# Kernel optimization log

Hardware: AMD Instinct MI355X
Metric: run time of the kernel (lower is better)

## Reference

```python
import jax, jax.numpy as jnp
import numpy as np

N = 50000
E = 800000
IN_C = 64
OUT_C = 64
EPS = 1 + 1e-06


def setup_inputs() -> dict:
    key = jax.random.key(0)
    ks = jax.random.split(key, 10)
    x = jax.random.normal(ks[0], (N, IN_C), dtype=jnp.float32)
    lower_indices = jax.random.randint(ks[1], (2, E), 0, N, dtype=jnp.int64)
    lower_values = jax.random.uniform(ks[2], (E,), dtype=jnp.float32)
    upper_indices = jax.random.randint(ks[3], (2, E), 0, N, dtype=jnp.int64)
    upper_values = jax.random.uniform(ks[4], (E,), dtype=jnp.float32)
    s = 1.0 / np.sqrt(IN_C)
    w_lower = jax.random.uniform(ks[5], (IN_C, OUT_C), jnp.float32, -s, s)
    a_lower = jax.random.uniform(ks[6], (2 * OUT_C,), jnp.float32, -s, s)
    w_upper = jax.random.uniform(ks[7], (IN_C, OUT_C), jnp.float32, -s, s)
    a_upper = jax.random.uniform(ks[8], (2 * OUT_C,), jnp.float32, -s, s)
    w_lin = jax.random.uniform(ks[9], (IN_C, OUT_C), jnp.float32, -s, s)
    return {
        "x": x,
        "lower_indices": lower_indices,
        "lower_values": lower_values,
        "upper_indices": upper_indices,
        "upper_values": upper_values,
        "w_lower": w_lower,
        "a_lower": a_lower,
        "w_upper": w_upper,
        "a_upper": a_upper,
        "w_lin": w_lin,
    }


def _att_conv(x, weight, att_w, indices, values):
    """TopoModelX base Conv with att=True.

    x_msg = x @ weight; per edge (i=target, j=source):
      alpha_e = elu(concat(x_msg[j], x_msg[i]) @ att_w) * nbhd_vals_e
    out[i] = sum_e alpha_e * x_msg[j]
    """
    xm = x @ weight                              # [N, out]
    i, j = indices[0], indices[1]                # target, source
    # concat(src, tgt) @ a == src @ a[:F] + tgt @ a[F:]; precompute per-node
    s_src = xm @ att_w[:OUT_C]                   # [N]
    s_tgt = xm @ att_w[OUT_C:]                   # [N]
    alpha = jax.nn.elu(s_src[j] + s_tgt[i]) * values   # [E]
    msg = alpha[:, None] * xm[j]                 # [E, out]
    return jax.ops.segment_sum(msg, i, num_segments=N)


def reference(x, lower_indices, lower_values, upper_indices, upper_values,
              w_lower, a_lower, w_upper, a_upper, w_lin):
    lower_x = _att_conv(x, w_lower, a_lower, lower_indices, lower_values)
    upper_x = _att_conv(x, w_upper, a_upper, upper_indices, upper_values)
    w_x = (x @ w_lin) * EPS
    # Aggregation(aggr_func='sum', update_func='relu')
    return jax.nn.relu(lower_x + upper_x + w_x)
```

## Files before the change

### kernel.cpp

```cpp
#include <hip/hip_runtime.h>
#include <hip/hip_bf16.h>
#include <math.h>

#define N_NODES 50000
#define N_EDGES 800000
#define C 64
#define EPS_F 1.000001f

#define CAPN 48
#define OVF_IDX 0
#define OMAX 4096
#define LOVF 64

#define RB_BITS 7
#define RBUK (1 << RB_BITS)
#define NBUCK (2 * N_NODES)
#define NREG ((NBUCK + RBUK - 1) >> RB_BITS)
#define RCAP 2560
#define EPB 4096
#define NP1 392
#define NPREB 784
#define NK1 (3 * NP1)

#define ZERON (1 + NREG)

typedef __attribute__((ext_vector_type(8))) unsigned short u16x8;

__device__ __forceinline__ unsigned short f2bf(float f) {
    unsigned u = __float_as_uint(f);
    return (unsigned short)((u + 0x7FFFu + ((u >> 16) & 1u)) >> 16);
}
__device__ __forceinline__ float bf2f(unsigned short b) {
    return __uint_as_float(((unsigned)b) << 16);
}

__global__ __launch_bounds__(512) void gemm_scatter_kernel(
    const float* __restrict__ x,
    const float* __restrict__ w_l, const float* __restrict__ a_l,
    const float* __restrict__ w_u, const float* __restrict__ a_u,
    const float* __restrict__ w_lin,
    const int* __restrict__ lidx, const float* __restrict__ lval,
    const int* __restrict__ uidx, const float* __restrict__ uval,
    unsigned short* __restrict__ xm_l, unsigned short* __restrict__ xm_u,
    float* __restrict__ xlin,
    float* __restrict__ ssl, float* __restrict__ stl,
    float* __restrict__ ssu, float* __restrict__ stu,
    int* __restrict__ cnt, uint2* __restrict__ rbuf, int2* __restrict__ ovf)
{
    const int b = blockIdx.x, t = threadIdx.x;
    __shared__ int hist[NREG];

    if (b % 3 == 0) {
        const int p = b / 3;
        int* __restrict__ rcur = cnt + 1;

        for (int s0 = t; s0 < NREG; s0 += 512) hist[s0] = 0;
        __syncthreads();

        unsigned lo[8];
        int bk[8];
        const int gbase = p * EPB + t;
#pragma unroll
        for (int k = 0; k < 8; ++k) {
            const int g = gbase + k * 512;
            bk[k] = -1;
            if (g < 2 * N_EDGES) {
                int i, j;
                float v;
                if (g < N_EDGES) {
                    i = lidx[g]; j = lidx[N_EDGES + g]; v = lval[g];
                    bk[k] = 2 * i;
                } else {
                    const int e = g - N_EDGES;
                    i = uidx[e]; j = uidx[N_EDGES + e]; v = uval[e];
                    bk[k] = 2 * i + 1;
                }
                lo[k] = ((unsigned)j << 16) | (unsigned)f2bf(v);
                atomicAdd(&hist[bk[k] >> RB_BITS], 1);
            }
        }
        __syncthreads();

        for (int cb = t; cb < NREG; cb += 512) {
            const int c = hist[cb];
            hist[cb] = c ? atomicAdd(&rcur[cb], c) : 0;
        }
        __syncthreads();

#pragma unroll
        for (int k = 0; k < 8; ++k) {
            if (bk[k] >= 0) {
                const int cb = bk[k] >> RB_BITS;
                const int slot = atomicAdd(&hist[cb], 1);
                if (slot < RCAP) {
                    rbuf[(size_t)cb * RCAP + slot] = make_uint2(lo[k], (unsigned)bk[k]);
                } else {
                    const int oi = atomicAdd(&cnt[OVF_IDX], 1);
                    if (oi < OMAX) ovf[oi] = make_int2(bk[k], (int)lo[k]);
                }
            }
        }
        return;
    }

    const int pid = b - b / 3 - 1;
    const int lane = t & 63;
    const int wvu = __builtin_amdgcn_readfirstlane(t >> 6);
    const int row0 = pid * 64 + wvu * 8;
    if (row0 >= N_NODES) return;

    const float* xr[8];
#pragma unroll
    for (int r = 0; r < 8; ++r) {
        int rr = row0 + r;
        if (rr >= N_NODES) rr = N_NODES - 1;
        xr[r] = x + (size_t)rr * C;
    }

    float acc_l[8] = {0,0,0,0,0,0,0,0};
    float acc_u[8] = {0,0,0,0,0,0,0,0};
    float acc_n[8] = {0,0,0,0,0,0,0,0};

#pragma unroll 1
    for (int kc = 0; kc < C; kc += 4) {
#pragma unroll
        for (int kk = 0; kk < 4; ++kk) {
            const int k = kc + kk;
            const float wl = w_l[k * C + lane];
            const float wu = w_u[k * C + lane];
            const float wn = w_lin[k * C + lane];
#pragma unroll
            for (int r = 0; r < 8; ++r) {
                const float xk = xr[r][k];
                acc_l[r] = fmaf(xk, wl, acc_l[r]);
                acc_u[r] = fmaf(xk, wu, acc_u[r]);
                acc_n[r] = fmaf(xk, wn, acc_n[r]);
            }
        }
    }

    const float als = a_l[lane], alt = a_l[C + lane];
    const float aus = a_u[lane], aut = a_u[C + lane];

#pragma unroll
    for (int r = 0; r < 8; ++r) {
        const int row = row0 + r;
        if (row < N_NODES) {
            xm_l[row * C + lane] = f2bf(acc_l[r]);
            xm_u[row * C + lane] = f2bf(acc_u[r]);
            xlin[row * C + lane] = acc_n[r] * EPS_F;

            float psl = acc_l[r] * als, ptl = acc_l[r] * alt;
            float psu = acc_u[r] * aus, ptu = acc_u[r] * aut;
#pragma unroll
            for (int o = 32; o >= 1; o >>= 1) {
                psl += __shfl_xor(psl, o);
                ptl += __shfl_xor(ptl, o);
                psu += __shfl_xor(psu, o);
                ptu += __shfl_xor(ptu, o);
            }
            if (lane == 0) {
                ssl[row] = psl; stl[row] = ptl;
                ssu[row] = psu; stu[row] = ptu;
            }
        }
    }
}

__global__ __launch_bounds__(512) void gather_kernel(
    const float* __restrict__ xlin,
    const int* __restrict__ cnt, const uint2* __restrict__ rbuf,
    const int2* __restrict__ ovf,
    const unsigned short* __restrict__ xm_l, const unsigned short* __restrict__ xm_u,
    const float* __restrict__ ssl, const float* __restrict__ stl,
    const float* __restrict__ ssu, const float* __restrict__ stu,
    float* __restrict__ out)
{
    const int cb = blockIdx.x;
    const int t = threadIdx.x;
    const int wv = t >> 6, lane = t & 63;
    const int sub8 = lane >> 3;
    const int cg = lane & 7;

    __shared__ unsigned lists[RBUK * CAPN];
    __shared__ int cur[RBUK];
    __shared__ int lovf_bk[LOVF];
    __shared__ unsigned lovf_rc[LOVF];
    __shared__ int lc;

    for (int s0 = t; s0 < RBUK; s0 += 512) cur[s0] = 0;
    if (t == 0) lc = 0;
    __syncthreads();

    const int n = min(cnt[1 + cb], RCAP);
    const uint2* __restrict__ rb = rbuf + (size_t)cb * RCAP;
    for (int r = t; r < n; r += 512) {
        const uint2 e = rb[r];
        const int local = (int)e.y & (RBUK - 1);
        const int rank = atomicAdd(&cur[local], 1);
        if (rank < CAPN) {
            lists[local * CAPN + rank] = e.x;
        } else {
            const int o = atomicAdd(&lc, 1);
            if (o < LOVF) { lovf_bk[o] = local; lovf_rc[o] = e.x; }
        }
    }
    __syncthreads();

    const int oc = min(cnt[OVF_IDX], OMAX);
    const int lc2 = min(lc, LOVF);

#pragma unroll 1
    for (int p = 0; p < 8; ++p) {
        const int q = wv * 8 + p;
        const int node = cb * 64 + q;
        if (node >= N_NODES) break;
        const int lA = 2 * q, lB = 2 * q + 1;
        const int lenA = min(cur[lA], CAPN);
        const int lenB = min(cur[lB], CAPN);
        const unsigned* __restrict__ lstA = lists + lA * CAPN;
        const unsigned* __restrict__ lstB = lists + lB * CAPN;

        const float stlN = stl[node];
        const float stuN = stu[node];

        float acc[8] = {0.f,0.f,0.f,0.f,0.f,0.f,0.f,0.f};
        int kA = 0, kB = 0;
        while ((kA < lenA) | (kB < lenB)) {
            const int iA = kA + sub8, iB = kB + sub8;
            const bool aA = iA < lenA, aB = iB < lenB;
            const unsigned rwA = lstA[aA ? iA : kA];
            const unsigned rwB = lstB[aB ? iB : kB];
            const int jA = aA ? (int)(rwA >> 16) : 0;
            const int jB = aB ? (int)(rwB >> 16) : 0;
            const float vA = aA ? bf2f((unsigned short)(rwA & 0xFFFFu)) : 0.f;
            const float vB = aB ? bf2f((unsigned short)(rwB & 0xFFFFu)) : 0.f;
            const float sA = ssl[jA] + stlN;
            const float sB = ssu[jB] + stuN;
            const float eA = (sA > 0.f) ? sA : expm1f(sA);
            const float eB = (sB > 0.f) ? sB : expm1f(sB);
            const float wA = eA * vA;
            const float wB = eB * vB;
            const u16x8 rowA = *(const u16x8*)(xm_l + jA * C + cg * 8);
            const u16x8 rowB = *(const u16x8*)(xm_u + jB * C + cg * 8);
#pragma unroll
            for (int c = 0; c < 8; ++c)
                acc[c] = fmaf(wA, bf2f(rowA[c]), acc[c]);
#pragma unroll
            for (int c = 0; c < 8; ++c)
                acc[c] = fmaf(wB, bf2f(rowB[c]), acc[c]);
            kA += (kA < lenA) ? 8 : 0;
            kB += (kB < lenB) ? 8 : 0;
        }

        for (int u = 0; u < oc; ++u) {
            const int2 e = ovf[u];
            if (e.x == 2 * node || e.x == 2 * node + 1) {
                const unsigned rw = (unsigned)e.y;
                const int j = (int)(rw >> 16);
                const float v = bf2f((unsigned short)(rw & 0xFFFFu));
                const int cv = e.x & 1;
                const float s = (cv ? ssu[j] : ssl[j]) + (cv ? stuN : stlN);
                const float el = (s > 0.f) ? s : expm1f(s);
                const float w = (sub8 == 0) ? el * v : 0.f;
                const unsigned short* xm = cv ? xm_u : xm_l;
                const u16x8 row = *(const u16x8*)(xm + j * C + cg * 8);
#pragma unroll
                for (int c = 0; c < 8; ++c)
                    acc[c] = fmaf(w, bf2f(row[c]), acc[c]);
            }
        }

        for (int u = 0; u < lc2; ++u) {
            const int bkl = lovf_bk[u];
            if (bkl == lA || bkl == lB) {
                const unsigned rw = lovf_rc[u];
                const int j = (int)(rw >> 16);
                const float v = bf2f((unsigned short)(rw & 0xFFFFu));
                const int cv = bkl & 1;
                const float s = (cv ? ssu[j] : ssl[j]) + (cv ? stuN : stlN);
                const float el = (s > 0.f) ? s : expm1f(s);
                const float w = (sub8 == 0) ? el * v : 0.f;
                const unsigned short* xm = cv ? xm_u : xm_l;
                const u16x8 row = *(const u16x8*)(xm + j * C + cg * 8);
#pragma unroll
                for (int c = 0; c < 8; ++c)
                    acc[c] = fmaf(w, bf2f(row[c]), acc[c]);
            }
        }

#pragma unroll
        for (int o = 8; o <= 32; o <<= 1)
#pragma unroll
            for (int c = 0; c < 8; ++c)
                acc[c] += __shfl_xor(acc[c], o);

        if (lane < 8) {
            const float* __restrict__ xl = xlin + (size_t)node * C + lane * 8;
            const float4 xa = *(const float4*)(xl);
            const float4 xb = *(const float4*)(xl + 4);
            float4 oa, ob;
            oa.x = fmaxf(acc[0] + xa.x, 0.f);
            oa.y = fmaxf(acc[1] + xa.y, 0.f);
            oa.z = fmaxf(acc[2] + xa.z, 0.f);
            oa.w = fmaxf(acc[3] + xa.w, 0.f);
            ob.x = fmaxf(acc[4] + xb.x, 0.f);
            ob.y = fmaxf(acc[5] + xb.y, 0.f);
            ob.z = fmaxf(acc[6] + xb.z, 0.f);
            ob.w = fmaxf(acc[7] + xb.w, 0.f);
            float* __restrict__ op = out + (size_t)node * C + lane * 8;
            *(float4*)(op) = oa;
            *(float4*)(op + 4) = ob;
        }
    }
}

extern "C" void kernel_launch(void* const* d_in, const int* in_sizes, int n_in,
                              void* d_out, int out_size, void* d_ws, size_t ws_size,
                              hipStream_t stream)
{
    const float* x          = (const float*)d_in[0];
    const int*   lower_idx  = (const int*)d_in[1];
    const float* lower_vals = (const float*)d_in[2];
    const int*   upper_idx  = (const int*)d_in[3];
    const float* upper_vals = (const float*)d_in[4];
    const float* w_lower    = (const float*)d_in[5];
    const float* a_lower    = (const float*)d_in[6];
    const float* w_upper    = (const float*)d_in[7];
    const float* a_upper    = (const float*)d_in[8];
    const float* w_lin      = (const float*)d_in[9];

    float* out = (float*)d_out;
    char* ws = (char*)d_ws;

    const size_t NC_F = (size_t)N_NODES * C * sizeof(float);
    const size_t NC_H = (size_t)N_NODES * C * sizeof(unsigned short);
    unsigned short* xm_l = (unsigned short*)ws;  ws += NC_H;
    unsigned short* xm_u = (unsigned short*)ws;  ws += NC_H;
    float* xlin = (float*)ws;                 ws += NC_F;
    float* ssl  = (float*)ws;                 ws += N_NODES * sizeof(float);
    float* stl  = (float*)ws;                 ws += N_NODES * sizeof(float);
    float* ssu  = (float*)ws;                 ws += N_NODES * sizeof(float);
    float* stu  = (float*)ws;                 ws += N_NODES * sizeof(float);
    int2* ovf   = (int2*)ws;                  ws += OMAX * sizeof(int2);
    uint2* rbuf = (uint2*)ws;                 ws += (size_t)NREG * RCAP * sizeof(uint2);
    int* cnt    = (int*)ws;                   ws += (size_t)(ZERON + 64) * sizeof(int);

    hipMemsetAsync(cnt, 0, ZERON * sizeof(int), stream);

    gemm_scatter_kernel<<<NK1, 512, 0, stream>>>(
        x, w_lower, a_lower, w_upper, a_upper, w_lin,
        lower_idx, lower_vals, upper_idx, upper_vals,
        xm_l, xm_u, xlin, ssl, stl, ssu, stu, cnt, rbuf, ovf);

    gather_kernel<<<NREG, 512, 0, stream>>>(
        xlin, cnt, rbuf, ovf, xm_l, xm_u, ssl, stl, ssu, stu, out);
}
```

Measured before the change: 183.6 us.

## Replace global atomic region buckets with per-block sorted chunks and offset directory

Each scatter block now sorts its edges locally by region using an in-block prefix scan and writes them to its own contiguous chunk. It also records a per-block directory of offsets and counts for each region. The gather kernel reads the directory column for its region and pulls the matching segments from all 392 chunks. This removes the global atomics, the memset, the fixed-capacity region buffers and the global overflow path. The cost is many small scattered segment reads per gather block plus the directory traffic.

```diff
diff --git a/kernel.cpp b/kernel.cpp
--- a/kernel.cpp
+++ b/kernel.cpp
@@ -8,21 +8,17 @@
 #define EPS_F 1.000001f
 
 #define CAPN 48
-#define OVF_IDX 0
-#define OMAX 4096
 #define LOVF 64
 
 #define RB_BITS 7
 #define RBUK (1 << RB_BITS)
 #define NBUCK (2 * N_NODES)
 #define NREG ((NBUCK + RBUK - 1) >> RB_BITS)
-#define RCAP 2560
+#define NREGP 1024
 #define EPB 4096
 #define NP1 392
 #define NPREB 784
 #define NK1 (3 * NP1)
-
-#define ZERON (1 + NREG)
 
 typedef __attribute__((ext_vector_type(8))) unsigned short u16x8;
 
@@ -45,16 +41,16 @@
     float* __restrict__ xlin,
     float* __restrict__ ssl, float* __restrict__ stl,
     float* __restrict__ ssu, float* __restrict__ stu,
-    int* __restrict__ cnt, uint2* __restrict__ rbuf, int2* __restrict__ ovf)
+    unsigned* __restrict__ dirT, uint2* __restrict__ rbuf)
 {
     const int b = blockIdx.x, t = threadIdx.x;
-    __shared__ int hist[NREG];
 
     if (b % 3 == 0) {
+        __shared__ int hist[NREGP];
+        __shared__ int psum[512];
         const int p = b / 3;
-        int* __restrict__ rcur = cnt + 1;
-
-        for (int s0 = t; s0 < NREG; s0 += 512) hist[s0] = 0;
+
+        hist[t] = 0; hist[t + 512] = 0;
         __syncthreads();
 
         unsigned lo[8];
@@ -81,23 +77,33 @@
         }
         __syncthreads();
 
-        for (int cb = t; cb < NREG; cb += 512) {
-            const int c = hist[cb];
-            hist[cb] = c ? atomicAdd(&rcur[cb], c) : 0;
-        }
-        __syncthreads();
-
+        const int a0 = hist[2 * t], a1 = hist[2 * t + 1];
+        psum[t] = a0 + a1;
+        __syncthreads();
+#pragma unroll
+        for (int off = 1; off < 512; off <<= 1) {
+            const int v = (t >= off) ? psum[t - off] : 0;
+            __syncthreads();
+            psum[t] += v;
+            __syncthreads();
+        }
+        const int base = (t == 0) ? 0 : psum[t - 1];
+        const int o0 = base, o1 = base + a0;
+
+        unsigned* __restrict__ drow = dirT + (size_t)p * NREGP;
+        drow[2 * t]     = ((unsigned)o0 << 16) | (unsigned)a0;
+        drow[2 * t + 1] = ((unsigned)o1 << 16) | (unsigned)a1;
+        __syncthreads();
+        hist[2 * t] = o0; hist[2 * t + 1] = o1;
+        __syncthreads();
+
+        uint2* __restrict__ chunk = rbuf + (size_t)p * EPB;
 #pragma unroll
         for (int k = 0; k < 8; ++k) {
             if (bk[k] >= 0) {
                 const int cb = bk[k] >> RB_BITS;
                 const int slot = atomicAdd(&hist[cb], 1);
-                if (slot < RCAP) {
-                    rbuf[(size_t)cb * RCAP + slot] = make_uint2(lo[k], (unsigned)bk[k]);
-                } else {
-                    const int oi = atomicAdd(&cnt[OVF_IDX], 1);
-                    if (oi < OMAX) ovf[oi] = make_int2(bk[k], (int)lo[k]);
-                }
+                chunk[slot] = make_uint2(lo[k], (unsigned)(bk[k] & (RBUK - 1)));
             }
         }
         return;
@@ -169,8 +175,7 @@
 
 __global__ __launch_bounds__(512) void gather_kernel(
     const float* __restrict__ xlin,
-    const int* __restrict__ cnt, const uint2* __restrict__ rbuf,
-    const int2* __restrict__ ovf,
+    const unsigned* __restrict__ dirT, const uint2* __restrict__ rbuf,
     const unsigned short* __restrict__ xm_l, const unsigned short* __restrict__ xm_u,
     const float* __restrict__ ssl, const float* __restrict__ stl,
     const float* __restrict__ ssu, const float* __restrict__ stu,
@@ -184,30 +189,36 @@
 
     __shared__ unsigned lists[RBUK * CAPN];
     __shared__ int cur[RBUK];
+    __shared__ unsigned dent[NP1];
     __shared__ int lovf_bk[LOVF];
     __shared__ unsigned lovf_rc[LOVF];
     __shared__ int lc;
 
     for (int s0 = t; s0 < RBUK; s0 += 512) cur[s0] = 0;
     if (t == 0) lc = 0;
+    for (int s0 = t; s0 < NP1; s0 += 512)
+        dent[s0] = dirT[(size_t)s0 * NREGP + cb];
     __syncthreads();
 
-    const int n = min(cnt[1 + cb], RCAP);
-    const uint2* __restrict__ rb = rbuf + (size_t)cb * RCAP;
-    for (int r = t; r < n; r += 512) {
-        const uint2 e = rb[r];
-        const int local = (int)e.y & (RBUK - 1);
-        const int rank = atomicAdd(&cur[local], 1);
-        if (rank < CAPN) {
-            lists[local * CAPN + rank] = e.x;
-        } else {
-            const int o = atomicAdd(&lc, 1);
-            if (o < LOVF) { lovf_bk[o] = local; lovf_rc[o] = e.x; }
+    for (int s = wv; s < NP1; s += 8) {
+        const unsigned de = dent[s];
+        const int n = (int)(de & 0xFFFFu);
+        if (n == 0) continue;
+        const uint2* __restrict__ seg = rbuf + (size_t)s * EPB + (de >> 16);
+        for (int l = lane; l < n; l += 64) {
+            const uint2 e = seg[l];
+            const int local = (int)e.y;
+            const int rank = atomicAdd(&cur[local], 1);
+            if (rank < CAPN) {
+                lists[local * CAPN + rank] = e.x;
+            } else {
+                const int o = atomicAdd(&lc, 1);
+                if (o < LOVF) { lovf_bk[o] = local; lovf_rc[o] = e.x; }
+            }
         }
     }
     __syncthreads();
 
-    const int oc = min(cnt[OVF_IDX], OMAX);
     const int lc2 = min(lc, LOVF);
 
 #pragma unroll 1
@@ -253,24 +264,6 @@
             kB += (kB < lenB) ? 8 : 0;
         }
 
-        for (int u = 0; u < oc; ++u) {
-            const int2 e = ovf[u];
-            if (e.x == 2 * node || e.x == 2 * node + 1) {
-                const unsigned rw = (unsigned)e.y;
-                const int j = (int)(rw >> 16);
-                const float v = bf2f((unsigned short)(rw & 0xFFFFu));
-                const int cv = e.x & 1;
-                const float s = (cv ? ssu[j] : ssl[j]) + (cv ? stuN : stlN);
-                const float el = (s > 0.f) ? s : expm1f(s);
-                const float w = (sub8 == 0) ? el * v : 0.f;
-                const unsigned short* xm = cv ? xm_u : xm_l;
-                const u16x8 row = *(const u16x8*)(xm + j * C + cg * 8);
-#pragma unroll
-                for (int c = 0; c < 8; ++c)
-                    acc[c] = fmaf(w, bf2f(row[c]), acc[c]);
-            }
-        }
-
         for (int u = 0; u < lc2; ++u) {
             const int bkl = lovf_bk[u];
             if (bkl == lA || bkl == lB) {
@@ -342,17 +335,14 @@
     float* stl  = (float*)ws;                 ws += N_NODES * sizeof(float);
     float* ssu  = (float*)ws;                 ws += N_NODES * sizeof(float);
     float* stu  = (float*)ws;                 ws += N_NODES * sizeof(float);
-    int2* ovf   = (int2*)ws;                  ws += OMAX * sizeof(int2);
-    uint2* rbuf = (uint2*)ws;                 ws += (size_t)NREG * RCAP * sizeof(uint2);
-    int* cnt    = (int*)ws;                   ws += (size_t)(ZERON + 64) * sizeof(int);
-
-    hipMemsetAsync(cnt, 0, ZERON * sizeof(int), stream);
+    uint2* rbuf = (uint2*)ws;                 ws += (size_t)NP1 * EPB * sizeof(uint2);
+    unsigned* dirT = (unsigned*)ws;           ws += (size_t)NP1 * NREGP * sizeof(unsigned);
 
     gemm_scatter_kernel<<<NK1, 512, 0, stream>>>(
         x, w_lower, a_lower, w_upper, a_upper, w_lin,
         lower_idx, lower_vals, upper_idx, upper_vals,
-        xm_l, xm_u, xlin, ssl, stl, ssu, stu, cnt, rbuf, ovf);
+        xm_l, xm_u, xlin, ssl, stl, ssu, stu, dirT, rbuf);
 
     gather_kernel<<<NREG, 512, 0, stream>>>(
-        xlin, cnt, rbuf, ovf, xm_l, xm_u, ssl, stl, ssu, stu, out);
-}
+        xlin, dirT, rbuf, xm_l, xm_u, ssl, stl, ssu, stu, out);
+}
```

Result: slower. 202.7 us (+10.4%).
